# Performance work log

Measured on AMD Instinct MI355X. Metric: run time of the kernel, lower is better.

Reference implementation:

```python
import jax, jax.numpy as jnp
import numpy as np

B, H, S, D = 2, 16, 2048, 64

def setup_inputs() -> dict:
    key = jax.random.key(0)
    kq, kk, kv = jax.random.split(key, 3)
    q = jax.random.normal(kq, (B, H, S, D), dtype=jnp.float32)
    k = jax.random.normal(kk, (B, H, S, D), dtype=jnp.float32)
    v = jax.random.normal(kv, (B, H, S, D), dtype=jnp.float32)
    # causal mask, broadcastable over batch and heads
    mask = jnp.tril(jnp.ones((S, S), dtype=bool))[None, None, :, :]
    return {"q": q, "k": k, "v": v, "mask": mask}

def reference(q, k, v, mask):
    d_k = q.shape[-1]
    # scores: [B, H, S, S]
    scores = jnp.einsum('bhqd,bhkd->bhqk', q, k) / (d_k ** 0.5)
    scores = jnp.where(mask, scores, -jnp.inf)
    probs = jax.nn.softmax(scores, axis=-1)  # numerically stable (max-subtracted)
    return jnp.einsum('bhqk,bhkd->bhqd', probs, v)
```

## Files before the change

kernel.cpp:

```cpp
#include <hip/hip_runtime.h>

#define S_LEN 2048
#define DHEAD 64
#define KVTILE 64
#define TBUF  18432
#define VOFF  9216
#define OPART 8704
#define LSOFF 34816

typedef float          f32x4  __attribute__((ext_vector_type(4)));
typedef float          f32x16 __attribute__((ext_vector_type(16)));
typedef unsigned int   u32x2  __attribute__((ext_vector_type(2)));
typedef unsigned int   u32x4  __attribute__((ext_vector_type(4)));
typedef __bf16         bf16x8 __attribute__((ext_vector_type(8)));

__device__ __forceinline__ unsigned int pack_bf16(float lo, float hi) {
  return __builtin_amdgcn_perm(__builtin_bit_cast(unsigned int, hi),
                               __builtin_bit_cast(unsigned int, lo),
                               0x07060302u);
}

__global__ __launch_bounds__(512, 2)
void attn_fwd_kernel(const float* __restrict__ qg_, const float* __restrict__ kg,
                     const float* __restrict__ vg, float* __restrict__ og)
{
  __shared__ __align__(16) unsigned char smem[36864];

  const int tid  = threadIdx.x;
  const int lane = tid & 63;
  const int l31  = lane & 31;
  const int hi   = lane >> 5;
  const int wid  = tid >> 6;
  const int qg   = wid & 3;
  const int par  = wid >> 2;

  const int bid = blockIdx.x;
  const int bh  = bid & 31;
  const int r   = bid >> 5;
  const int qt2 = (r < 8) ? r : 23 - r;

  const int q0w = qt2 * 128 + qg * 32;
  const int tb  = 2 * qt2 + (qg >> 1);

  const float* qp = qg_ + (size_t)bh * S_LEN * DHEAD;
  const float* kp = kg  + (size_t)bh * S_LEN * DHEAD;
  const float* vp = vg  + (size_t)bh * S_LEN * DHEAD;
  float*       op = og  + (size_t)bh * S_LEN * DHEAD;

  const int sh   = tid >> 8;
  const int stid = tid & 255;
  const int krow = stid >> 2;
  const int kd0  = (stid & 3) * 16;
  const int va   = ((stid >> 6) << 2) | (stid & 3);
  const int vm   = (stid >> 2) & 15;

  f32x4 kxr[4];
  f32x4 vxr[4];

  auto load_k = [&](int kv0) {
    #pragma unroll
    for (int i = 0; i < 4; ++i)
      kxr[i] = *reinterpret_cast<const f32x4*>(
          kp + (size_t)(kv0 + krow) * DHEAD + kd0 + 4 * i);
  };
  auto load_v = [&](int kv0) {
    #pragma unroll
    for (int j = 0; j < 4; ++j)
      vxr[j] = *reinterpret_cast<const f32x4*>(
          vp + (size_t)(kv0 + 4 * va + j) * DHEAD + 4 * vm);
  };

  auto stage_kv = [&]() {
    unsigned char* kb = smem + sh * TBUF;
    u32x4 w0, w1;
    w0[0] = pack_bf16(kxr[0][0], kxr[0][1]); w0[1] = pack_bf16(kxr[0][2], kxr[0][3]);
    w0[2] = pack_bf16(kxr[1][0], kxr[1][1]); w0[3] = pack_bf16(kxr[1][2], kxr[1][3]);
    w1[0] = pack_bf16(kxr[2][0], kxr[2][1]); w1[1] = pack_bf16(kxr[2][2], kxr[2][3]);
    w1[2] = pack_bf16(kxr[3][0], kxr[3][1]); w1[3] = pack_bf16(kxr[3][2], kxr[3][3]);
    *reinterpret_cast<u32x4*>(kb + krow * 144 + kd0 * 2)      = w0;
    *reinterpret_cast<u32x4*>(kb + krow * 144 + kd0 * 2 + 16) = w1;
    unsigned char* vb = kb + VOFF;
    #pragma unroll
    for (int c = 0; c < 4; ++c) {
      const int d = 4 * vm + c;
      u32x2 w;
      w[0] = pack_bf16(vxr[0][c], vxr[1][c]);
      w[1] = pack_bf16(vxr[2][c], vxr[3][c]);
      const int s16 = (va >> 1) ^ ((d >> 1) & 7);
      *reinterpret_cast<u32x2*>(vb + d * 144 + s16 * 16 + (va & 1) * 8) = w;
    }
  };

  const float qscale = 0.125f * 1.44269504f;
  bf16x8 qf[4];
  #pragma unroll
  for (int dstep = 0; dstep < 4; ++dstep) {
    const f32x4* src = reinterpret_cast<const f32x4*>(
        qp + (size_t)(q0w + l31) * DHEAD + dstep * 16 + hi * 8);
    f32x4 x0 = src[0];
    f32x4 x1 = src[1];
    u32x4 qw;
    qw[0] = pack_bf16(x0[0] * qscale, x0[1] * qscale);
    qw[1] = pack_bf16(x0[2] * qscale, x0[3] * qscale);
    qw[2] = pack_bf16(x1[0] * qscale, x1[1] * qscale);
    qw[3] = pack_bf16(x1[2] * qscale, x1[3] * qscale);
    qf[dstep] = __builtin_bit_cast(bf16x8, qw);
  }

  f32x16 oacc[2] = {};
  float lsum = 0.f;

  load_k(sh * KVTILE);
  load_v(sh * KVTILE);
  stage_kv();
  __syncthreads();

  unsigned char* kbase = smem + par * TBUF;
  unsigned char* vbase = kbase + VOFF;

  auto process_half = [&](int a, int limit) {
    f32x16 sacc = {};
    __builtin_amdgcn_s_setprio(1);
    #pragma unroll
    for (int dstep = 0; dstep < 4; ++dstep) {
      bf16x8 kf = *reinterpret_cast<const bf16x8*>(
          kbase + (a * 32 + l31) * 144 + dstep * 32 + hi * 16);
      sacc = __builtin_amdgcn_mfma_f32_32x32x16_bf16(kf, qf[dstep], sacc, 0, 0, 0);
    }
    __builtin_amdgcn_s_setprio(0);

    unsigned int w0[4], w1[4];
    #pragma unroll
    for (int g = 0; g < 4; ++g) {
      float p[4];
      #pragma unroll
      for (int i = 0; i < 4; ++i) {
        const int kva = a * 32 + 8 * g + 4 * hi + i;
        float pv = __builtin_amdgcn_exp2f(sacc[4 * g + i]);
        if (kva > limit) pv = 0.f;
        p[i] = pv;
      }
      lsum += (p[0] + p[1]) + (p[2] + p[3]);
      w0[g] = pack_bf16(p[0], p[1]);
      w1[g] = pack_bf16(p[2], p[3]);
    }

    bf16x8 pfrag[2];
    #pragma unroll
    for (int b = 0; b < 2; ++b) {
      const unsigned int x0 = w0[2 * b], y0 = w0[2 * b + 1];
      const unsigned int x1 = w1[2 * b], y1 = w1[2 * b + 1];
      const unsigned int sx0 = (unsigned int)__shfl_xor((int)x0, 32, 64);
      const unsigned int sy0 = (unsigned int)__shfl_xor((int)y0, 32, 64);
      const unsigned int sx1 = (unsigned int)__shfl_xor((int)x1, 32, 64);
      const unsigned int sy1 = (unsigned int)__shfl_xor((int)y1, 32, 64);
      u32x4 f;
      f[0] = hi ? sy0 : x0;
      f[1] = hi ? sy1 : x1;
      f[2] = hi ? y0 : sx0;
      f[3] = hi ? y1 : sx1;
      pfrag[b] = __builtin_bit_cast(bf16x8, f);
    }

    __builtin_amdgcn_s_setprio(1);
    #pragma unroll
    for (int dh = 0; dh < 2; ++dh) {
      const int d = dh * 32 + l31;
      #pragma unroll
      for (int b = 0; b < 2; ++b) {
        const int s16 = (2 * (2 * a + b) + hi) ^ ((d >> 1) & 7);
        bf16x8 vf = *reinterpret_cast<const bf16x8*>(vbase + d * 144 + s16 * 16);
        oacc[dh] = __builtin_amdgcn_mfma_f32_32x32x16_bf16(vf, pfrag[b], oacc[dh], 0, 0, 0);
      }
    }
    __builtin_amdgcn_s_setprio(0);
  };

  for (int s = 0; s <= qt2; ++s) {
    const bool more = (s < qt2);
    if (more) load_k((2 * s + 2 + sh) * KVTILE);

    const int t_w = 2 * s + par;
    if (t_w <= tb) {
      const int limit = q0w + l31 - t_w * KVTILE;
      process_half(0, limit);
      process_half(1, limit);
    }

    if (more) load_v((2 * s + 2 + sh) * KVTILE);

    __syncthreads();
    if (more) { stage_kv(); __syncthreads(); }
  }

  float ls2 = lsum + __shfl_xor(lsum, 32, 64);
  if (par == 0) {
    unsigned char* ob = smem + qg * OPART + l31 * 272;
    #pragma unroll
    for (int dh = 0; dh < 2; ++dh)
      #pragma unroll
      for (int m = 0; m < 4; ++m) {
        f32x4 o;
        #pragma unroll
        for (int i = 0; i < 4; ++i) o[i] = oacc[dh][4 * m + i];
        *reinterpret_cast<f32x4*>(ob + (dh * 32 + 8 * m + 4 * hi) * 4) = o;
      }
    if (hi == 0)
      *reinterpret_cast<float*>(smem + LSOFF + qg * 128 + l31 * 4) = ls2;
  }
  __syncthreads();
  if (par == 1) {
    const float ltot = ls2 +
        *reinterpret_cast<const float*>(smem + LSOFF + qg * 128 + l31 * 4);
    const float rl = 1.0f / ltot;
    unsigned char* ob = smem + qg * OPART + l31 * 272;
    #pragma unroll
    for (int dh = 0; dh < 2; ++dh)
      #pragma unroll
      for (int m = 0; m < 4; ++m) {
        const f32x4 part = *reinterpret_cast<const f32x4*>(
            ob + (dh * 32 + 8 * m + 4 * hi) * 4);
        f32x4 o;
        #pragma unroll
        for (int i = 0; i < 4; ++i) o[i] = (oacc[dh][4 * m + i] + part[i]) * rl;
        *reinterpret_cast<f32x4*>(
            op + (size_t)(q0w + l31) * DHEAD + dh * 32 + 8 * m + 4 * hi) = o;
      }
  }
}

extern "C" void kernel_launch(void* const* d_in, const int* in_sizes, int n_in,
                              void* d_out, int out_size, void* d_ws, size_t ws_size,
                              hipStream_t stream) {
  const float* q = (const float*)d_in[0];
  const float* k = (const float*)d_in[1];
  const float* v = (const float*)d_in[2];
  float* out = (float*)d_out;

  dim3 grid(512);
  dim3 block(512);
  attn_fwd_kernel<<<grid, block, 0, stream>>>(q, k, v, out);
}
```

Measured before the change: 52.99 us.

## Double-buffer K/V LDS tiles with XOR swizzle and drop per-iteration barrier

Splits the LDS staging area into two buffers per parity so the next K/V tile is written to the alternate buffer while the current one is consumed. This removes one of the two __syncthreads per iteration. The V global load moves between the two process_half calls to overlap its latency with compute. It also replaces the padded 144-byte row stride with a 128-byte stride plus XOR swizzle to avoid LDS bank conflicts without padding. LDS grows to 64 KB per block, which at 2 blocks per CU may limit occupancy on a 160 KB LDS CU.

```diff
diff --git a/kernel.cpp b/kernel.cpp
--- a/kernel.cpp
+++ b/kernel.cpp
@@ -3,8 +3,9 @@
 #define S_LEN 2048
 #define DHEAD 64
 #define KVTILE 64
-#define TBUF  18432
-#define VOFF  9216
+#define TBUF  16384
+#define VOFF  8192
+#define PSTRIDE 32768
 #define OPART 8704
 #define LSOFF 34816
 
@@ -24,7 +25,7 @@
 void attn_fwd_kernel(const float* __restrict__ qg_, const float* __restrict__ kg,
                      const float* __restrict__ vg, float* __restrict__ og)
 {
-  __shared__ __align__(16) unsigned char smem[36864];
+  __shared__ __align__(16) unsigned char smem[65536];
 
   const int tid  = threadIdx.x;
   const int lane = tid & 63;
@@ -50,7 +51,8 @@
   const int sh   = tid >> 8;
   const int stid = tid & 255;
   const int krow = stid >> 2;
-  const int kd0  = (stid & 3) * 16;
+  const int kc2  = stid & 3;
+  const int kd0  = kc2 * 16;
   const int va   = ((stid >> 6) << 2) | (stid & 3);
   const int vm   = (stid >> 2) & 15;
 
@@ -70,15 +72,16 @@
           vp + (size_t)(kv0 + 4 * va + j) * DHEAD + 4 * vm);
   };
 
-  auto stage_kv = [&]() {
-    unsigned char* kb = smem + sh * TBUF;
+  auto stage_kv = [&](int buf) {
+    unsigned char* kb = smem + sh * PSTRIDE + buf * TBUF;
+    const int k7 = krow & 7;
     u32x4 w0, w1;
     w0[0] = pack_bf16(kxr[0][0], kxr[0][1]); w0[1] = pack_bf16(kxr[0][2], kxr[0][3]);
     w0[2] = pack_bf16(kxr[1][0], kxr[1][1]); w0[3] = pack_bf16(kxr[1][2], kxr[1][3]);
     w1[0] = pack_bf16(kxr[2][0], kxr[2][1]); w1[1] = pack_bf16(kxr[2][2], kxr[2][3]);
     w1[2] = pack_bf16(kxr[3][0], kxr[3][1]); w1[3] = pack_bf16(kxr[3][2], kxr[3][3]);
-    *reinterpret_cast<u32x4*>(kb + krow * 144 + kd0 * 2)      = w0;
-    *reinterpret_cast<u32x4*>(kb + krow * 144 + kd0 * 2 + 16) = w1;
+    *reinterpret_cast<u32x4*>(kb + krow * 128 + (((kc2 << 1)    ) ^ k7) * 16) = w0;
+    *reinterpret_cast<u32x4*>(kb + krow * 128 + (((kc2 << 1) + 1) ^ k7) * 16) = w1;
     unsigned char* vb = kb + VOFF;
     #pragma unroll
     for (int c = 0; c < 4; ++c) {
@@ -86,8 +89,8 @@
       u32x2 w;
       w[0] = pack_bf16(vxr[0][c], vxr[1][c]);
       w[1] = pack_bf16(vxr[2][c], vxr[3][c]);
-      const int s16 = (va >> 1) ^ ((d >> 1) & 7);
-      *reinterpret_cast<u32x2*>(vb + d * 144 + s16 * 16 + (va & 1) * 8) = w;
+      *reinterpret_cast<u32x2*>(
+          vb + d * 128 + (((va >> 1) ^ (d & 7)) * 16) + (va & 1) * 8) = w;
     }
   };
 
@@ -112,19 +115,16 @@
 
   load_k(sh * KVTILE);
   load_v(sh * KVTILE);
-  stage_kv();
+  stage_kv(0);
   __syncthreads();
 
-  unsigned char* kbase = smem + par * TBUF;
-  unsigned char* vbase = kbase + VOFF;
-
-  auto process_half = [&](int a, int limit) {
+  auto process_half = [&](int a, int limit, unsigned char* kbase, unsigned char* vbase) {
     f32x16 sacc = {};
     __builtin_amdgcn_s_setprio(1);
     #pragma unroll
     for (int dstep = 0; dstep < 4; ++dstep) {
       bf16x8 kf = *reinterpret_cast<const bf16x8*>(
-          kbase + (a * 32 + l31) * 144 + dstep * 32 + hi * 16);
+          kbase + (a * 32 + l31) * 128 + (((dstep << 1) + hi) ^ (l31 & 7)) * 16);
       sacc = __builtin_amdgcn_mfma_f32_32x32x16_bf16(kf, qf[dstep], sacc, 0, 0, 0);
     }
     __builtin_amdgcn_s_setprio(0);
@@ -168,8 +168,8 @@
       const int d = dh * 32 + l31;
       #pragma unroll
       for (int b = 0; b < 2; ++b) {
-        const int s16 = (2 * (2 * a + b) + hi) ^ ((d >> 1) & 7);
-        bf16x8 vf = *reinterpret_cast<const bf16x8*>(vbase + d * 144 + s16 * 16);
+        bf16x8 vf = *reinterpret_cast<const bf16x8*>(
+            vbase + d * 128 + ((((2 * a + b) << 1) + hi) ^ (l31 & 7)) * 16);
         oacc[dh] = __builtin_amdgcn_mfma_f32_32x32x16_bf16(vf, pfrag[b], oacc[dh], 0, 0, 0);
       }
     }
@@ -177,20 +177,24 @@
   };
 
   for (int s = 0; s <= qt2; ++s) {
+    const int cur = s & 1;
     const bool more = (s < qt2);
+    unsigned char* kbase = smem + par * PSTRIDE + cur * TBUF;
+    unsigned char* vbase = kbase + VOFF;
+
     if (more) load_k((2 * s + 2 + sh) * KVTILE);
 
     const int t_w = 2 * s + par;
-    if (t_w <= tb) {
-      const int limit = q0w + l31 - t_w * KVTILE;
-      process_half(0, limit);
-      process_half(1, limit);
-    }
-
+    const bool act = (t_w <= tb);
+    const int limit = q0w + l31 - t_w * KVTILE;
+
+    if (act) process_half(0, limit, kbase, vbase);
     if (more) load_v((2 * s + 2 + sh) * KVTILE);
+    if (act) process_half(1, limit, kbase, vbase);
+
+    if (more) stage_kv(cur ^ 1);
 
     __syncthreads();
-    if (more) { stage_kv(); __syncthreads(); }
   }
 
   float ls2 = lsum + __shfl_xor(lsum, 32, 64);
```

New measurement: 46.76 us. 11.7% less time.
